# Kernel tuning notes

Measured on AMD Instinct MI355X. Metric: run time of the kernel, lower is better.

## Reference

```python
import jax, jax.numpy as jnp
import numpy as np

# Model dims (match init_kwargs / input_specs)
T, N, E, F_IN, F_OUT, BW = 16, 50000, 131072, 64, 64, 3


def setup_inputs() -> dict:
    key = jax.random.key(0)
    ks = jax.random.split(key, 6)
    x = jax.random.normal(ks[0], (T, N, F_IN), dtype=jnp.float32)
    M = jax.random.normal(ks[1], (T, T), dtype=jnp.float32)
    adj_rows = jax.random.randint(ks[2], (T, E), 0, N, dtype=jnp.int32)
    adj_cols = jax.random.randint(ks[3], (T, E), 0, N, dtype=jnp.int32)
    adj_vals = jax.random.uniform(ks[4], (T, E), dtype=jnp.float32)
    lim = float(np.sqrt(6.0 / (F_IN + F_OUT)))  # xavier_uniform
    weight = jax.random.uniform(ks[5], (F_IN, F_OUT), minval=-lim, maxval=lim, dtype=jnp.float32)
    return {"x": x, "M": M, "adj_vals": adj_vals, "weight": weight,
            "adj_rows": adj_rows, "adj_cols": adj_cols}


def _spmm(vals, rows, cols, x):
    # COO sparse [N,N] @ dense [N,F]: gather source rows, scatter-add to dest rows.
    return jax.ops.segment_sum(vals[:, None] * x[cols], rows, num_segments=x.shape[0])


def reference(x, M, adj_vals, weight, adj_rows, adj_cols):
    Tn, Nn, F = x.shape
    # Xt = M @ X (full M, as in compute_AtXt)
    Xt = (M @ x.reshape(Tn, -1)).reshape(Tn, Nn, F)
    k_idx = jnp.arange(Tn)
    AtXt = jnp.zeros((Tn, Nn, F), dtype=x.dtype)
    # Banded combination: At[k] = sum_{d=0}^{BW-1, k-d>=0} M[k, k-d] * A[k-d]
    # so At[k] @ Xt[k] = sum_d M[k,k-d] * (A[k-d] @ Xt[k])  -- avoids materializing At.
    for d in range(BW):
        j = k_idx - d
        valid = j >= 0
        jc = jnp.maximum(j, 0)
        w = jnp.where(valid, M[k_idx, jc], 0.0)  # [T] banded weights
        contrib = jax.vmap(_spmm)(adj_vals[jc], adj_rows[jc], adj_cols[jc], Xt)  # [T,N,F]
        AtXt = AtXt + w[:, None, None] * contrib
    # dropout is identity in eval mode; final dense projection
    return AtXt @ weight  # [T, N, F_OUT]
```

## Files before the change

### kernel.cpp

```cpp
#include <hip/hip_runtime.h>

#define TT 16
#define NN 50000
#define FF 64
#define EE 131072
#define NEDGE (TT*EE)
#define RPB 32
#define NRANGE ((NN + RPB - 1) / RPB)
#define NSUB 8
#define BCAP 256
#define NBUCK (NRANGE*NSUB)
#define SLOTS (NSUB*BCAP)
#define EMAX 1791
#define TAILI (EMAX*2)
#define K1BLKS 1563
#define APPBLKS (NEDGE/256)

typedef __attribute__((ext_vector_type(8))) short bf16x8;
typedef __attribute__((ext_vector_type(4))) short bf16x4;
typedef __attribute__((ext_vector_type(4))) float f32x4;
typedef __attribute__((ext_vector_type(2))) int   i32x2;
typedef __attribute__((ext_vector_type(2))) unsigned u32x2;

__device__ __forceinline__ unsigned pack2bf(float a, float b) {
    unsigned ua = __float_as_uint(a) + 0x8000u;
    unsigned ub = __float_as_uint(b) + 0x8000u;
    return __builtin_amdgcn_perm(ub, ua, 0x07060302u);
}
__device__ __forceinline__ float lo16f(unsigned u) { return __uint_as_float(u << 16); }
__device__ __forceinline__ float hi16f(unsigned u) { return __uint_as_float(u & 0xFFFF0000u); }

union U8 { unsigned u[4]; bf16x8 v; };
union U4 { unsigned u[2]; bf16x4 v; };

__device__ __forceinline__ f32x4 mfma16x16x16bf16(bf16x4 a, bf16x4 b, f32x4 c) {
#if __has_builtin(__builtin_amdgcn_mfma_f32_16x16x16bf16_1k)
    return __builtin_amdgcn_mfma_f32_16x16x16bf16_1k(a, b, c, 0, 0, 0);
#elif __has_builtin(__builtin_amdgcn_mfma_f32_16x16x16_bf16)
    return __builtin_amdgcn_mfma_f32_16x16x16_bf16(a, b, c, 0, 0, 0);
#else
    f32x4 d;
    asm volatile("v_mfma_f32_16x16x16_bf16 %0, %1, %2, %3\n\ts_nop 7\n\ts_nop 7"
                 : "=&v"(d) : "v"(a), "v"(b), "v"(c));
    return d;
#endif
}

__global__ __launch_bounds__(256) void k1_append(
    const float* __restrict__ x, const float* __restrict__ M,
    const float* __restrict__ W, unsigned short* __restrict__ Yt,
    const int* __restrict__ rows, const int* __restrict__ cols,
    const float* __restrict__ vals, int* __restrict__ bcnt,
    i32x2* __restrict__ btmp)
{
    if (blockIdx.x < K1BLKS) {
        const int tid  = threadIdx.x;
        const int wid  = tid >> 6;
        const int lane = tid & 63;
        const int col  = lane & 15;
        const int grp  = lane >> 4;

        bf16x8 bw[2][4];
#pragma unroll
        for (int q = 0; q < 2; ++q)
#pragma unroll
            for (int t = 0; t < 4; ++t) {
                U8 w8;
#pragma unroll
                for (int p = 0; p < 4; ++p)
                    w8.u[p] = pack2bf(W[(q*32 + grp*8 + 2*p)*FF + t*16 + col],
                                      W[(q*32 + grp*8 + 2*p + 1)*FF + t*16 + col]);
                bw[q][t] = w8.v;
            }

        U4 m4;
        m4.u[0] = pack2bf(M[col*16 + grp*4 + 0], M[col*16 + grp*4 + 1]);
        m4.u[1] = pack2bf(M[col*16 + grp*4 + 2], M[col*16 + grp*4 + 3]);
        const bf16x4 mf = m4.v;

        const f32x4 zero = {0.f, 0.f, 0.f, 0.f};
        const int wave_id = blockIdx.x*4 + wid;
        const size_t lane_off = (size_t)col*NN*FF + grp*8;

#pragma unroll
        for (int it = 0; it < 4; ++it) {
            const int node = wave_id*8 + it*2;
            if (node < NN) {
                const float* xa = x + lane_off + (size_t)node*FF;
                f32x4 va0 = __builtin_nontemporal_load(reinterpret_cast<const f32x4*>(xa));
                f32x4 va1 = __builtin_nontemporal_load(reinterpret_cast<const f32x4*>(xa + 4));
                f32x4 va2 = __builtin_nontemporal_load(reinterpret_cast<const f32x4*>(xa + 32));
                f32x4 va3 = __builtin_nontemporal_load(reinterpret_cast<const f32x4*>(xa + 36));
                f32x4 vb0 = __builtin_nontemporal_load(reinterpret_cast<const f32x4*>(xa + 64));
                f32x4 vb1 = __builtin_nontemporal_load(reinterpret_cast<const f32x4*>(xa + 68));
                f32x4 vb2 = __builtin_nontemporal_load(reinterpret_cast<const f32x4*>(xa + 96));
                f32x4 vb3 = __builtin_nontemporal_load(reinterpret_cast<const f32x4*>(xa + 100));

#pragma unroll
                for (int n2 = 0; n2 < 2; ++n2) {
                    U8 a0, a1;
                    if (n2 == 0) {
                        a0.u[0] = pack2bf(va0[0], va0[1]); a0.u[1] = pack2bf(va0[2], va0[3]);
                        a0.u[2] = pack2bf(va1[0], va1[1]); a0.u[3] = pack2bf(va1[2], va1[3]);
                        a1.u[0] = pack2bf(va2[0], va2[1]); a1.u[1] = pack2bf(va2[2], va2[3]);
                        a1.u[2] = pack2bf(va3[0], va3[1]); a1.u[3] = pack2bf(va3[2], va3[3]);
                    } else {
                        a0.u[0] = pack2bf(vb0[0], vb0[1]); a0.u[1] = pack2bf(vb0[2], vb0[3]);
                        a0.u[2] = pack2bf(vb1[0], vb1[1]); a0.u[3] = pack2bf(vb1[2], vb1[3]);
                        a1.u[0] = pack2bf(vb2[0], vb2[1]); a1.u[1] = pack2bf(vb2[2], vb2[3]);
                        a1.u[2] = pack2bf(vb3[0], vb3[1]); a1.u[3] = pack2bf(vb3[2], vb3[3]);
                    }
                    f32x4 acc[4];
#pragma unroll
                    for (int t = 0; t < 4; ++t) acc[t] = zero;
#pragma unroll
                    for (int t = 0; t < 4; ++t)
                        acc[t] = __builtin_amdgcn_mfma_f32_16x16x32_bf16(a0.v, bw[0][t], acc[t], 0, 0, 0);
#pragma unroll
                    for (int t = 0; t < 4; ++t)
                        acc[t] = __builtin_amdgcn_mfma_f32_16x16x32_bf16(a1.v, bw[1][t], acc[t], 0, 0, 0);
#pragma unroll
                    for (int t = 0; t < 4; ++t) {
                        U4 pb;
                        pb.u[0] = pack2bf(acc[t][0], acc[t][1]);
                        pb.u[1] = pack2bf(acc[t][2], acc[t][3]);
                        f32x4 y = mfma16x16x16bf16(pb.v, mf, zero);
                        u32x2 st;
                        st[0] = pack2bf(y[0], y[1]);
                        st[1] = pack2bf(y[2], y[3]);
                        *reinterpret_cast<u32x2*>(Yt + (size_t)(node + n2)*1024 + col*64 + t*16 + grp*4) = st;
                    }
                }
            }
        }
    } else {
        const int i = (blockIdx.x - K1BLKS)*256 + threadIdx.x;
        const int r = __builtin_nontemporal_load(rows + i);
        const int j = i >> 17;
        const int b = (r >> 5)*NSUB + (blockIdx.x & 7);
        const int pos = atomicAdd(&bcnt[b], 1);
        if (pos < BCAP) {
            i32x2 e;
            e[0] = __builtin_nontemporal_load(cols + i) | (((r & 31)*16 + j) << 16);
            e[1] = __float_as_int(__builtin_nontemporal_load(vals + i));
            btmp[(size_t)b*BCAP + pos] = e;
        }
    }
}

__global__ __launch_bounds__(256) void sort_kernel(
    const int* __restrict__ bcnt, i32x2* __restrict__ btmp)
{
    __shared__ i32x2 sbuf[SLOTS];
    __shared__ int scnt[512], soff[512], scur[512], pscan[256];

    const int tid = threadIdx.x;
    const int blk = blockIdx.x;
    i32x2* region = btmp + (size_t)blk*SLOTS;

    scnt[tid] = 0; scnt[tid + 256] = 0;
    __syncthreads();

    int bc[NSUB]; i32x2 ent[NSUB];
#pragma unroll
    for (int s = 0; s < NSUB; ++s) {
        int c = bcnt[blk*NSUB + s];
        bc[s] = c < BCAP ? c : BCAP;
    }
#pragma unroll
    for (int s = 0; s < NSUB; ++s)
        if (tid < bc[s]) {
            ent[s] = region[s*BCAP + tid];
            atomicAdd(&scnt[((unsigned)ent[s][0]) >> 16], 1);
        }
    __syncthreads();

    const int a0 = scnt[2*tid], a1 = scnt[2*tid + 1];
    const int ps = a0 + a1;
    pscan[tid] = ps;
    __syncthreads();
    for (int o = 1; o < 256; o <<= 1) {
        int v = (tid >= o) ? pscan[tid - o] : 0;
        __syncthreads();
        pscan[tid] += v;
        __syncthreads();
    }
    const int excl = pscan[tid] - ps;
    soff[2*tid] = excl;      soff[2*tid + 1] = excl + a0;
    scur[2*tid] = excl;      scur[2*tid + 1] = excl + a0;
    __syncthreads();

#pragma unroll
    for (int s = 0; s < NSUB; ++s)
        if (tid < bc[s]) {
            const int key = ((unsigned)ent[s][0]) >> 16;
            const int pos = atomicAdd(&scur[key], 1);
            i32x2 se; se[0] = ent[s][0] & 0xFFFF; se[1] = ent[s][1];
            sbuf[pos] = se;
        }
    __syncthreads();

    const int total = soff[511] + scnt[511];
    const int lim = total < EMAX ? total : EMAX;
    for (int i = tid; i < lim; i += 256) region[i] = sbuf[i];
    int* tail = (int*)region + TAILI;
    tail[tid] = soff[tid];
    tail[tid + 256] = soff[tid + 256];
    if (tid == 0) tail[512] = lim;
}

template<int J>
__device__ __forceinline__ void k2_batch(int p0, int nj, int sbase, int esub, int fq,
    const i32x2* eb, const unsigned short* __restrict__ Yt,
    const float* __restrict__ M, f32x4* acc)
{
    const int p = p0 + esub;
    const bool act = p < nj;
    const int li = act ? (sbase + p) : 0;
    const i32x2 ent = eb[li];
    const float v = act ? __int_as_float(ent[1]) : 0.f;
    const int node = act ? ent[0] : 0;
    const unsigned short* yb = Yt + (size_t)node*1024 + J*64 + fq*4;
    {
        const u32x2 uv = *reinterpret_cast<const u32x2*>(yb);
        const float wv = M[J*17] * v;
        acc[J][0] = fmaf(wv, lo16f(uv[0]), acc[J][0]);
        acc[J][1] = fmaf(wv, hi16f(uv[0]), acc[J][1]);
        acc[J][2] = fmaf(wv, lo16f(uv[1]), acc[J][2]);
        acc[J][3] = fmaf(wv, hi16f(uv[1]), acc[J][3]);
    }
    if constexpr (J < 15) {
        const u32x2 uv = *reinterpret_cast<const u32x2*>(yb + 64);
        const float wv = M[J*17 + 16] * v;
        acc[J+1][0] = fmaf(wv, lo16f(uv[0]), acc[J+1][0]);
        acc[J+1][1] = fmaf(wv, hi16f(uv[0]), acc[J+1][1]);
        acc[J+1][2] = fmaf(wv, lo16f(uv[1]), acc[J+1][2]);
        acc[J+1][3] = fmaf(wv, hi16f(uv[1]), acc[J+1][3]);
    }
    if constexpr (J < 14) {
        const u32x2 uv = *reinterpret_cast<const u32x2*>(yb + 128);
        const float wv = M[J*17 + 32] * v;
        acc[J+2][0] = fmaf(wv, lo16f(uv[0]), acc[J+2][0]);
        acc[J+2][1] = fmaf(wv, hi16f(uv[0]), acc[J+2][1]);
        acc[J+2][2] = fmaf(wv, lo16f(uv[1]), acc[J+2][2]);
        acc[J+2][3] = fmaf(wv, hi16f(uv[1]), acc[J+2][3]);
    }
}

__global__ __launch_bounds__(256) void k2_gather(
    const unsigned short* __restrict__ Yt, const float* __restrict__ M,
    const i32x2* __restrict__ btmp, float* __restrict__ out)
{
    __shared__ i32x2 ebuf[4][128];
    const int tid  = threadIdx.x;
    const int wid  = tid >> 6;
    const int lane = tid & 63;
    const int esub = lane >> 4;
    const int fq   = lane & 15;
    const int r   = blockIdx.x*4 + wid;
    const int blk = r >> 5;
    const int rl  = r & 31;

    const i32x2* region = btmp + (size_t)blk*SLOTS;
    const int* tail = (const int*)region + TAILI;
    int o_l = 0;
    if (lane < 17) o_l = tail[rl*16 + lane];
    int off[17];
#pragma unroll
    for (int j = 0; j < 17; ++j) off[j] = __builtin_amdgcn_readlane(o_l, j);
    int ntot = off[16] - off[0];
    ntot = ntot < 128 ? ntot : 128;
    const i32x2* rowsrc = region + off[0];

    i32x2* eb = ebuf[wid];
    if (lane < ntot)      eb[lane]      = rowsrc[lane];
    if (lane + 64 < ntot) eb[lane + 64] = rowsrc[lane + 64];

    int c[16], sb[16];
#pragma unroll
    for (int j = 0; j < 16; ++j) {
        c[j]  = off[j+1] - off[j];
        sb[j] = off[j] - off[0];
    }

    f32x4 acc[16];
#pragma unroll
    for (int k = 0; k < 16; ++k) acc[k] = (f32x4){0.f, 0.f, 0.f, 0.f};

#define P1(J) k2_batch<J>(0, c[J], sb[J], esub, fq, eb, Yt, M, acc);
    P1(0)  P1(1)  P1(2)  P1(3)  P1(4)  P1(5)  P1(6)  P1(7)
    P1(8)  P1(9)  P1(10) P1(11) P1(12) P1(13) P1(14) P1(15)
#undef P1
#define P2(J) for (int p0 = 4; p0 < c[J]; p0 += 4) \
        k2_batch<J>(p0, c[J], sb[J], esub, fq, eb, Yt, M, acc);
    P2(0)  P2(1)  P2(2)  P2(3)  P2(4)  P2(5)  P2(6)  P2(7)
    P2(8)  P2(9)  P2(10) P2(11) P2(12) P2(13) P2(14) P2(15)
#undef P2

#pragma unroll
    for (int k = 0; k < 16; ++k) {
#pragma unroll
        for (int u = 0; u < 4; ++u) {
            acc[k][u] += __shfl_xor(acc[k][u], 16);
            acc[k][u] += __shfl_xor(acc[k][u], 32);
        }
    }
    if (esub == 0) {
#pragma unroll
        for (int k = 0; k < 16; ++k) {
            *reinterpret_cast<f32x4*>(out + ((size_t)k*NN + r)*FF + fq*4) = acc[k];
        }
    }
}

extern "C" void kernel_launch(void* const* d_in, const int* in_sizes, int n_in,
                              void* d_out, int out_size, void* d_ws, size_t ws_size,
                              hipStream_t stream) {
    (void)in_sizes; (void)n_in; (void)out_size; (void)ws_size;
    const float* x     = (const float*)d_in[0];
    const float* M     = (const float*)d_in[1];
    const float* avals = (const float*)d_in[2];
    const float* W     = (const float*)d_in[3];
    const int*   arows = (const int*)d_in[4];
    const int*   acols = (const int*)d_in[5];
    float* out = (float*)d_out;

    char* ws = (char*)d_ws;
    size_t o = 0;
    unsigned short* Yt = (unsigned short*)(ws + o); o += (size_t)TT*NN*FF*2;
    o = (o + 255) & ~(size_t)255;
    int* bcnt = (int*)(ws + o); o += (size_t)NBUCK*4;  o = (o + 255) & ~(size_t)255;
    i32x2* btmp = (i32x2*)(ws + o);

    (void)hipMemsetAsync(bcnt, 0, (size_t)NBUCK*4, stream);
    hipLaunchKernelGGL(k1_append, dim3(K1BLKS + APPBLKS), dim3(256), 0, stream,
                       x, M, W, Yt, arows, acols, avals, bcnt, btmp);
    hipLaunchKernelGGL(sort_kernel, dim3(NRANGE), dim3(256), 0, stream, bcnt, btmp);
    hipLaunchKernelGGL(k2_gather, dim3(12500), dim3(256), 0, stream, Yt, M, btmp, out);
}
```

Measured before the change: 340.3 us.

## Apply temporal mix before weight projection and prefetch next node's inputs

Reorders the dense stage so the T×T temporal mix M is applied to x first and the 64×64 weight projection second, using 16x16x16 bf16 MFMAs per 16-feature chunk. Each wave now walks 8 nodes one at a time, software-prefetching the next node's x values into registers while the current one computes. Global loads become scalar strided reads across the time dimension instead of vector nontemporal loads, and stores become 2-byte scalar writes. The order of rounding to bf16 changes, and load coalescing may get worse.

Result: faster. 328.9 us (-3.4%).

```diff
diff --git a/kernel.cpp b/kernel.cpp
--- a/kernel.cpp
+++ b/kernel.cpp
@@ -27,6 +27,9 @@
     unsigned ub = __float_as_uint(b) + 0x8000u;
     return __builtin_amdgcn_perm(ub, ua, 0x07060302u);
 }
+__device__ __forceinline__ unsigned short f2bf_rhu(float a) {
+    return (unsigned short)((__float_as_uint(a) + 0x8000u) >> 16);
+}
 __device__ __forceinline__ float lo16f(unsigned u) { return __uint_as_float(u << 16); }
 __device__ __forceinline__ float hi16f(unsigned u) { return __uint_as_float(u & 0xFFFF0000u); }
 
@@ -60,17 +63,17 @@
         const int col  = lane & 15;
         const int grp  = lane >> 4;
 
-        bf16x8 bw[2][4];
-#pragma unroll
-        for (int q = 0; q < 2; ++q)
+        bf16x4 bw[4][4];
+#pragma unroll
+        for (int c = 0; c < 4; ++c)
 #pragma unroll
             for (int t = 0; t < 4; ++t) {
-                U8 w8;
-#pragma unroll
-                for (int p = 0; p < 4; ++p)
-                    w8.u[p] = pack2bf(W[(q*32 + grp*8 + 2*p)*FF + t*16 + col],
-                                      W[(q*32 + grp*8 + 2*p + 1)*FF + t*16 + col]);
-                bw[q][t] = w8.v;
+                U4 w4;
+                w4.u[0] = pack2bf(W[(c*16 + grp*4 + 0)*FF + t*16 + col],
+                                  W[(c*16 + grp*4 + 1)*FF + t*16 + col]);
+                w4.u[1] = pack2bf(W[(c*16 + grp*4 + 2)*FF + t*16 + col],
+                                  W[(c*16 + grp*4 + 3)*FF + t*16 + col]);
+                bw[c][t] = w4.v;
             }
 
         U4 m4;
@@ -79,60 +82,61 @@
         const bf16x4 mf = m4.v;
 
         const f32x4 zero = {0.f, 0.f, 0.f, 0.f};
-        const int wave_id = blockIdx.x*4 + wid;
-        const size_t lane_off = (size_t)col*NN*FF + grp*8;
-
-#pragma unroll
-        for (int it = 0; it < 4; ++it) {
-            const int node = wave_id*8 + it*2;
+        const int base_node = (blockIdx.x*4 + wid)*8;
+
+        f32x4 cur[4], nxt[4];
+#define LOADX(nd, dst)                                                        \
+        {                                                                     \
+            const int ndc = (nd) < NN ? (nd) : NN - 1;                        \
+            _Pragma("unroll")                                                 \
+            for (int c = 0; c < 4; ++c) {                                     \
+                _Pragma("unroll")                                             \
+                for (int j = 0; j < 4; ++j)                                   \
+                    dst[c][j] = x[(size_t)(grp*4 + j)*NN*FF                   \
+                                  + (size_t)ndc*FF + c*16 + col];             \
+            }                                                                 \
+        }
+
+        LOADX(base_node, cur)
+#pragma unroll
+        for (int it = 0; it < 8; ++it) {
+            const int node = base_node + it;
+            if (it < 7) LOADX(node + 1, nxt)
+
+            f32x4 xtT[4];
+#pragma unroll
+            for (int c = 0; c < 4; ++c) {
+                U4 xa;
+                xa.u[0] = pack2bf(cur[c][0], cur[c][1]);
+                xa.u[1] = pack2bf(cur[c][2], cur[c][3]);
+                xtT[c] = mfma16x16x16bf16(xa.v, mf, zero);
+            }
+
+            f32x4 acc[4];
+#pragma unroll
+            for (int t = 0; t < 4; ++t) acc[t] = zero;
+#pragma unroll
+            for (int c = 0; c < 4; ++c) {
+                U4 a4;
+                a4.u[0] = pack2bf(xtT[c][0], xtT[c][1]);
+                a4.u[1] = pack2bf(xtT[c][2], xtT[c][3]);
+#pragma unroll
+                for (int t = 0; t < 4; ++t)
+                    acc[t] = mfma16x16x16bf16(a4.v, bw[c][t], acc[t]);
+            }
+
             if (node < NN) {
-                const float* xa = x + lane_off + (size_t)node*FF;
-                f32x4 va0 = __builtin_nontemporal_load(reinterpret_cast<const f32x4*>(xa));
-                f32x4 va1 = __builtin_nontemporal_load(reinterpret_cast<const f32x4*>(xa + 4));
-                f32x4 va2 = __builtin_nontemporal_load(reinterpret_cast<const f32x4*>(xa + 32));
-                f32x4 va3 = __builtin_nontemporal_load(reinterpret_cast<const f32x4*>(xa + 36));
-                f32x4 vb0 = __builtin_nontemporal_load(reinterpret_cast<const f32x4*>(xa + 64));
-                f32x4 vb1 = __builtin_nontemporal_load(reinterpret_cast<const f32x4*>(xa + 68));
-                f32x4 vb2 = __builtin_nontemporal_load(reinterpret_cast<const f32x4*>(xa + 96));
-                f32x4 vb3 = __builtin_nontemporal_load(reinterpret_cast<const f32x4*>(xa + 100));
-
-#pragma unroll
-                for (int n2 = 0; n2 < 2; ++n2) {
-                    U8 a0, a1;
-                    if (n2 == 0) {
-                        a0.u[0] = pack2bf(va0[0], va0[1]); a0.u[1] = pack2bf(va0[2], va0[3]);
-                        a0.u[2] = pack2bf(va1[0], va1[1]); a0.u[3] = pack2bf(va1[2], va1[3]);
-                        a1.u[0] = pack2bf(va2[0], va2[1]); a1.u[1] = pack2bf(va2[2], va2[3]);
-                        a1.u[2] = pack2bf(va3[0], va3[1]); a1.u[3] = pack2bf(va3[2], va3[3]);
-                    } else {
-                        a0.u[0] = pack2bf(vb0[0], vb0[1]); a0.u[1] = pack2bf(vb0[2], vb0[3]);
-                        a0.u[2] = pack2bf(vb1[0], vb1[1]); a0.u[3] = pack2bf(vb1[2], vb1[3]);
-                        a1.u[0] = pack2bf(vb2[0], vb2[1]); a1.u[1] = pack2bf(vb2[2], vb2[3]);
-                        a1.u[2] = pack2bf(vb3[0], vb3[1]); a1.u[3] = pack2bf(vb3[2], vb3[3]);
-                    }
-                    f32x4 acc[4];
-#pragma unroll
-                    for (int t = 0; t < 4; ++t) acc[t] = zero;
-#pragma unroll
-                    for (int t = 0; t < 4; ++t)
-                        acc[t] = __builtin_amdgcn_mfma_f32_16x16x32_bf16(a0.v, bw[0][t], acc[t], 0, 0, 0);
-#pragma unroll
-                    for (int t = 0; t < 4; ++t)
-                        acc[t] = __builtin_amdgcn_mfma_f32_16x16x32_bf16(a1.v, bw[1][t], acc[t], 0, 0, 0);
-#pragma unroll
-                    for (int t = 0; t < 4; ++t) {
-                        U4 pb;
-                        pb.u[0] = pack2bf(acc[t][0], acc[t][1]);
-                        pb.u[1] = pack2bf(acc[t][2], acc[t][3]);
-                        f32x4 y = mfma16x16x16bf16(pb.v, mf, zero);
-                        u32x2 st;
-                        st[0] = pack2bf(y[0], y[1]);
-                        st[1] = pack2bf(y[2], y[3]);
-                        *reinterpret_cast<u32x2*>(Yt + (size_t)(node + n2)*1024 + col*64 + t*16 + grp*4) = st;
-                    }
-                }
+#pragma unroll
+                for (int t = 0; t < 4; ++t)
+#pragma unroll
+                    for (int r = 0; r < 4; ++r)
+                        Yt[(size_t)node*1024 + (grp*4 + r)*64 + t*16 + col] =
+                            f2bf_rhu(acc[t][r]);
             }
-        }
+#pragma unroll
+            for (int c = 0; c < 4; ++c) cur[c] = nxt[c];
+        }
+#undef LOADX
     } else {
         const int i = (blockIdx.x - K1BLKS)*256 + threadIdx.x;
         const int r = __builtin_nontemporal_load(rows + i);
```
